# Optimization experiments

Measured on AMD Instinct MI355X. Metric: run time of the kernel, lower is better.

## Reference

```python
import jax, jax.numpy as jnp
import numpy as np

B, Q, S, U = 65536, 128, 8, 32  # batch, n_slices, slice_length (1024/128), hidden units


def setup_inputs() -> dict:
    key = jax.random.key(0)
    k1, k2, k3 = jax.random.split(key, 3)
    x = jax.random.normal(k1, (B, 1, 1, Q * S), dtype=jnp.float32)
    # Per-slice 2-layer MLP params: Dense(U, elu) then Dense(1), one set per slice.
    W1 = jax.random.normal(k2, (Q, S, U), dtype=jnp.float32) * (1.0 / np.sqrt(S))
    b1 = jnp.zeros((Q, U), dtype=jnp.float32)
    W2 = jax.random.normal(k3, (Q, U, 1), dtype=jnp.float32) * (1.0 / np.sqrt(U))
    b2 = jnp.zeros((Q, 1), dtype=jnp.float32)
    return {"x": x, "W1": W1, "b1": b1, "W2": W2, "b2": b2}


def reference(x, W1, b1, W2, b2):
    # x: (B,1,1,C) -> (B, Q, S); note: BN layers in the original __init__ are
    # never used in call(), so the forward is purely the per-slice MLPs.
    b = x.shape[0]
    xs = jnp.reshape(x, (b, Q, S))
    # All 128 per-slice Dense layers fused into one batched GEMM.
    h = jax.nn.elu(jnp.einsum('bqs,qsu->bqu', xs, W1) + b1)  # (B,Q,U)
    out = jnp.einsum('bqu,quo->bqo', h, W2) + b2              # (B,Q,1)
    return jnp.reshape(out, (b, Q))                           # concat over q -> (B,Q)
```

## Files before the change

### kernel.cpp

```cpp
#include <hip/hip_runtime.h>

#define Q    128
#define S    8
#define U    32
#define QW   8
#define TROWS 64
#define RPB  1024
#define NTILE (RPB / TROWS)
#define RSTRIDE 272
#define ZOFF (TROWS * RSTRIDE)
#define OSS  20

typedef __attribute__((ext_vector_type(8)))  __bf16 bf16x8;
typedef __attribute__((ext_vector_type(16))) float  f32x16;
typedef __attribute__((ext_vector_type(2)))  float  f32x2;

__device__ inline unsigned short f2bf(float f) {
    unsigned int u = __float_as_uint(f);
    u += 0x7FFF + ((u >> 16) & 1);
    return (unsigned short)(u >> 16);
}

__device__ inline unsigned int cvt_pk_bf16(float lo, float hi) {
    unsigned int r;
    asm("v_cvt_pk_bf16_f32 %0, %1, %2" : "=v"(r) : "v"(lo), "v"(hi));
    return r;
}

__global__ void prep_kernel(const float* __restrict__ W1, const float* __restrict__ b1,
                            const float* __restrict__ W2, const float* __restrict__ b2,
                            unsigned short* __restrict__ W1T,
                            float* __restrict__ b1F, float* __restrict__ w2F,
                            float* __restrict__ b2F)
{
    const int q = blockIdx.x, t = threadIdx.x;
    const int u = t & 31, s = t >> 5;
    W1T[(q * 32 + u) * 8 + s] = f2bf(W1[(q * 8 + s) * 32 + u]);
    if (t < 32) {
        int reg = t & 15, hh = t >> 4;
        int uu  = (reg & 3) + 8 * (reg >> 2) + 4 * hh;
        b1F[(q * 2 + hh) * 16 + reg] = b1[q * 32 + uu] + 1.0f;
        w2F[(q * 2 + hh) * 16 + reg] = W2[q * 32 + uu];
    }
    if (t == 0) {
        float sw = 0.f;
        for (int uu = 0; uu < 32; ++uu) sw += W2[q * 32 + uu];
        b2F[q] = b2[q] - sw;
    }
}

__global__ __launch_bounds__(256)
__attribute__((amdgpu_waves_per_eu(3, 4)))
void divenc_wreg(const float* __restrict__ x,
                 const unsigned short* __restrict__ W1T,
                 const float* __restrict__ b1F,
                 const float* __restrict__ w2F,
                 const float* __restrict__ b2F,
                 float* __restrict__ out, int B)
{
    __shared__ __align__(16) unsigned char xs[TROWS * RSTRIDE + 16];
    __shared__ __align__(16) float os[TROWS * OSS];

    const int t    = threadIdx.x;
    const int lane = t & 63;
    const int wv   = __builtin_amdgcn_readfirstlane(t >> 6);
    const int bl   = lane & 31;
    const int h    = lane >> 5;
    const bool lo  = (lane < 32);

    const int bid   = blockIdx.x;
    const int qb    = (bid & 15) * QW;
    const int rbase = (bid >> 4) * RPB;
    const int rmax  = B - 1;

    if (t == 0) *(uint4*)(xs + ZOFF) = uint4{0, 0, 0, 0};

    const int qA = qb + wv * 2, qB = qA + 1;
    const uint4  axA  = *(const uint4*)(W1T + ((size_t)qA * 32 + bl) * 8);
    const uint4  axB  = *(const uint4*)(W1T + ((size_t)qB * 32 + bl) * 8);
    const f32x16 cinA = *(const f32x16*)(b1F + ((size_t)qA * 2 + h) * 16);
    const f32x16 cinB = *(const f32x16*)(b1F + ((size_t)qB * 2 + h) * 16);
    const f32x16 wrA  = *(const f32x16*)(w2F + ((size_t)qA * 2 + h) * 16);
    const f32x16 wrB  = *(const f32x16*)(w2F + ((size_t)qB * 2 + h) * 16);
    const float  b2A  = b2F[qA], b2B = b2F[qB];

    const f32x2 l2e2  = 1.44269504088896f;
    const f32x2 nl2e2 = -1.44269504088896f;
    const f32x2 zero2 = 0.0f;

    const int row0 = t >> 3,          qr0 = t & 7;
    const int row1 = (t + 256) >> 3,  qr1 = t & 7;
    float4 pa0, pb0, pa1, pb1;

#define LOADT(T) {                                                                   \
    int r0_ = rbase + (T) * TROWS + row0; if (r0_ > rmax) r0_ = rmax;                \
    int r1_ = rbase + (T) * TROWS + row1; if (r1_ > rmax) r1_ = rmax;                \
    const float4* p0_ = (const float4*)(x + (size_t)r0_ * (Q * S)                    \
                                          + (size_t)(qb + qr0) * S);                 \
    const float4* p1_ = (const float4*)(x + (size_t)r1_ * (Q * S)                    \
                                          + (size_t)(qb + qr1) * S);                 \
    pa0 = p0_[0]; pb0 = p0_[1];                                                      \
    pa1 = p1_[0]; pb1 = p1_[1]; }

#define WRITET() {                                                                   \
    uint4 w0_, w1_;                                                                  \
    w0_.x = cvt_pk_bf16(pa0.x, pa0.y); w0_.y = cvt_pk_bf16(pa0.z, pa0.w);            \
    w0_.z = cvt_pk_bf16(pb0.x, pb0.y); w0_.w = cvt_pk_bf16(pb0.z, pb0.w);            \
    w1_.x = cvt_pk_bf16(pa1.x, pa1.y); w1_.y = cvt_pk_bf16(pa1.z, pa1.w);            \
    w1_.z = cvt_pk_bf16(pb1.x, pb1.y); w1_.w = cvt_pk_bf16(pb1.z, pb1.w);            \
    *(uint4*)(xs + row0 * RSTRIDE + qr0 * 16) = w0_;                                 \
    *(uint4*)(xs + row1 * RSTRIDE + qr1 * 16) = w1_; }

#define EL2(CC, J, WR, ACC) {                                                        \
    f32x2 v_; v_.x = CC[2*(J)]; v_.y = CC[2*(J)+1];                                  \
    f32x2 w2v; w2v.x = WR[2*(J)]; w2v.y = WR[2*(J)+1];                               \
    f32x2 f_ = __builtin_elementwise_fma(v_, l2e2, nl2e2);                           \
    f_ = __builtin_elementwise_min(f_, zero2);                                       \
    f32x2 e_; e_.x = __builtin_amdgcn_exp2f(f_.x);                                   \
    e_.y = __builtin_amdgcn_exp2f(f_.y);                                             \
    f32x2 r_ = __builtin_elementwise_max(v_, e_);                                    \
    ACC = __builtin_elementwise_fma(r_, w2v, ACC); }

#define COMP(AX, CIN, WR, B2, QR) {                                                  \
    const int xoff = bl * RSTRIDE + (QR) * 16;                                       \
    uint4 bx0 = *(const uint4*)(xs + (lo ? xoff                : ZOFF));             \
    uint4 bx1 = *(const uint4*)(xs + (lo ? xoff + 32 * RSTRIDE : ZOFF));             \
    f32x16 cc0 = __builtin_amdgcn_mfma_f32_32x32x16_bf16(                            \
        __builtin_bit_cast(bf16x8, AX), __builtin_bit_cast(bf16x8, bx0),             \
        CIN, 0, 0, 0);                                                               \
    f32x16 cc1 = __builtin_amdgcn_mfma_f32_32x32x16_bf16(                            \
        __builtin_bit_cast(bf16x8, AX), __builtin_bit_cast(bf16x8, bx1),             \
        CIN, 0, 0, 0);                                                               \
    f32x2 acc0 = 0.0f, acc1 = 0.0f;                                                  \
    EL2(cc0, 0, WR, acc0) EL2(cc0, 1, WR, acc0) EL2(cc0, 2, WR, acc0)                \
    EL2(cc0, 3, WR, acc0) EL2(cc0, 4, WR, acc0) EL2(cc0, 5, WR, acc0)                \
    EL2(cc0, 6, WR, acc0) EL2(cc0, 7, WR, acc0)                                      \
    EL2(cc1, 0, WR, acc1) EL2(cc1, 1, WR, acc1) EL2(cc1, 2, WR, acc1)                \
    EL2(cc1, 3, WR, acc1) EL2(cc1, 4, WR, acc1) EL2(cc1, 5, WR, acc1)                \
    EL2(cc1, 6, WR, acc1) EL2(cc1, 7, WR, acc1)                                      \
    float a0 = acc0.x + acc0.y;                                                      \
    float a1 = acc1.x + acc1.y;                                                      \
    a0 += __shfl_xor(a0, 32);                                  \
    a1 += __shfl_xor(a1, 32);                                                        \
    if (lo) {                                                                        \
        os[bl * OSS + (QR)]        = a0 + (B2);                                      \
        os[(bl + 32) * OSS + (QR)] = a1 + (B2);                                      \
    } }

    LOADT(0) WRITET()

    #pragma unroll 1
    for (int tile = 0; tile < NTILE; ++tile) {
        __syncthreads();

        if (tile + 1 < NTILE) LOADT(tile + 1)

        COMP(axA, cinA, wrA, b2A, wv * 2)
        COMP(axB, cinB, wrB, b2B, wv * 2 + 1)

        __syncthreads();

        if (t < 128) {
            int row = t >> 1, c = t & 1;
            float4 o = *(const float4*)&os[row * OSS + c * 4];
            int r = rbase + tile * TROWS + row;
            if (r < B)
                *(float4*)(out + (size_t)r * Q + qb + c * 4) = o;
        }

        if (tile + 1 < NTILE) WRITET()
    }
#undef LOADT
#undef WRITET
#undef EL2
#undef COMP
}

extern "C" void kernel_launch(void* const* d_in, const int* in_sizes, int n_in,
                              void* d_out, int out_size, void* d_ws, size_t ws_size,
                              hipStream_t stream) {
    const float* x  = (const float*)d_in[0];
    const float* W1 = (const float*)d_in[1];
    const float* b1 = (const float*)d_in[2];
    const float* W2 = (const float*)d_in[3];
    const float* b2 = (const float*)d_in[4];
    float* out = (float*)d_out;

    unsigned short* W1T = (unsigned short*)d_ws;
    float*          b1F = (float*)((char*)d_ws + 65536);
    float*          w2F = (float*)((char*)d_ws + 81920);
    float*          b2F = (float*)((char*)d_ws + 98304);

    const int B = in_sizes[0] / (Q * S);
    const int nblocks = ((B + RPB - 1) / RPB) * (Q / QW);

    hipLaunchKernelGGL(prep_kernel, dim3(Q), dim3(256), 0, stream,
                       W1, b1, W2, b2, W1T, b1F, w2F, b2F);
    hipLaunchKernelGGL(divenc_wreg, dim3(nblocks), dim3(256), 0, stream,
                       x, W1T, b1F, w2F, b2F, out, B);
}
```

Measured before the change: 82.16 us.

## Double-buffer x and output tiles in LDS to drop one barrier per tile

The staged input tile and output tile in shared memory become double-buffered, so the next tile can be written while the current one is computed and the previous tile's outputs are stored. This removes the second __syncthreads per iteration and defers each output store by one iteration. The LDS row stride also shrinks from 272 to 144 bytes, which keeps the total footprint modest but may change bank-conflict behaviour on the MFMA operand reads.

```diff
diff --git a/kernel.cpp b/kernel.cpp
--- a/kernel.cpp
+++ b/kernel.cpp
@@ -7,9 +7,11 @@
 #define TROWS 64
 #define RPB  1024
 #define NTILE (RPB / TROWS)
-#define RSTRIDE 272
-#define ZOFF (TROWS * RSTRIDE)
-#define OSS  20
+#define RSTRIDE 144
+#define XSBUF (TROWS * RSTRIDE)
+#define ZOFF  (2 * XSBUF)
+#define OSS   20
+#define OSBUF (TROWS * OSS)
 
 typedef __attribute__((ext_vector_type(8)))  __bf16 bf16x8;
 typedef __attribute__((ext_vector_type(16))) float  f32x16;
@@ -58,8 +60,8 @@
                  const float* __restrict__ b2F,
                  float* __restrict__ out, int B)
 {
-    __shared__ __align__(16) unsigned char xs[TROWS * RSTRIDE + 16];
-    __shared__ __align__(16) float os[TROWS * OSS];
+    __shared__ __align__(16) unsigned char xs[2 * XSBUF + 16];
+    __shared__ __align__(16) float os[2 * OSBUF];
 
     const int t    = threadIdx.x;
     const int lane = t & 63;
@@ -102,14 +104,14 @@
     pa0 = p0_[0]; pb0 = p0_[1];                                                      \
     pa1 = p1_[0]; pb1 = p1_[1]; }
 
-#define WRITET() {                                                                   \
+#define WRITET(BUF) {                                                                \
     uint4 w0_, w1_;                                                                  \
     w0_.x = cvt_pk_bf16(pa0.x, pa0.y); w0_.y = cvt_pk_bf16(pa0.z, pa0.w);            \
     w0_.z = cvt_pk_bf16(pb0.x, pb0.y); w0_.w = cvt_pk_bf16(pb0.z, pb0.w);            \
     w1_.x = cvt_pk_bf16(pa1.x, pa1.y); w1_.y = cvt_pk_bf16(pa1.z, pa1.w);            \
     w1_.z = cvt_pk_bf16(pb1.x, pb1.y); w1_.w = cvt_pk_bf16(pb1.z, pb1.w);            \
-    *(uint4*)(xs + row0 * RSTRIDE + qr0 * 16) = w0_;                                 \
-    *(uint4*)(xs + row1 * RSTRIDE + qr1 * 16) = w1_; }
+    *(uint4*)(xs + (BUF) * XSBUF + row0 * RSTRIDE + qr0 * 16) = w0_;                 \
+    *(uint4*)(xs + (BUF) * XSBUF + row1 * RSTRIDE + qr1 * 16) = w1_; }
 
 #define EL2(CC, J, WR, ACC) {                                                        \
     f32x2 v_; v_.x = CC[2*(J)]; v_.y = CC[2*(J)+1];                                  \
@@ -121,8 +123,8 @@
     f32x2 r_ = __builtin_elementwise_max(v_, e_);                                    \
     ACC = __builtin_elementwise_fma(r_, w2v, ACC); }
 
-#define COMP(AX, CIN, WR, B2, QR) {                                                  \
-    const int xoff = bl * RSTRIDE + (QR) * 16;                                       \
+#define COMP(AX, CIN, WR, B2, QR, RBUF, OSP) {                                       \
+    const int xoff = (RBUF) + bl * RSTRIDE + (QR) * 16;                              \
     uint4 bx0 = *(const uint4*)(xs + (lo ? xoff                : ZOFF));             \
     uint4 bx1 = *(const uint4*)(xs + (lo ? xoff + 32 * RSTRIDE : ZOFF));             \
     f32x16 cc0 = __builtin_amdgcn_mfma_f32_32x32x16_bf16(                            \
@@ -143,37 +145,43 @@
     a0 += __shfl_xor(a0, 32);                                  \
     a1 += __shfl_xor(a1, 32);                                                        \
     if (lo) {                                                                        \
-        os[bl * OSS + (QR)]        = a0 + (B2);                                      \
-        os[(bl + 32) * OSS + (QR)] = a1 + (B2);                                      \
+        os[(OSP) + bl * OSS + (QR)]        = a0 + (B2);                              \
+        os[(OSP) + (bl + 32) * OSS + (QR)] = a1 + (B2);                              \
     } }
 
-    LOADT(0) WRITET()
+#define STORE(T, OSP) {                                                              \
+    if (t < 128) {                                                                   \
+        int row_ = t >> 1, c_ = t & 1;                                               \
+        float4 o_ = *(const float4*)&os[(OSP) + row_ * OSS + c_ * 4];                \
+        int r_ = rbase + (T) * TROWS + row_;                                         \
+        if (r_ < B)                                                                  \
+            *(float4*)(out + (size_t)r_ * Q + qb + c_ * 4) = o_;                     \
+    } }
+
+    LOADT(0) WRITET(0)
 
     #pragma unroll 1
     for (int tile = 0; tile < NTILE; ++tile) {
         __syncthreads();
+        const int rbuf = (tile & 1) * XSBUF;
+        const int osp  = (tile & 1) * OSBUF;
+        const int psp  = ((tile & 1) ^ 1) * OSBUF;
 
         if (tile + 1 < NTILE) LOADT(tile + 1)
-
-        COMP(axA, cinA, wrA, b2A, wv * 2)
-        COMP(axB, cinB, wrB, b2B, wv * 2 + 1)
-
-        __syncthreads();
-
-        if (t < 128) {
-            int row = t >> 1, c = t & 1;
-            float4 o = *(const float4*)&os[row * OSS + c * 4];
-            int r = rbase + tile * TROWS + row;
-            if (r < B)
-                *(float4*)(out + (size_t)r * Q + qb + c * 4) = o;
-        }
-
-        if (tile + 1 < NTILE) WRITET()
+        if (tile > 0)         STORE(tile - 1, psp)
+
+        COMP(axA, cinA, wrA, b2A, wv * 2,     rbuf, osp)
+        COMP(axB, cinB, wrB, b2B, wv * 2 + 1, rbuf, osp)
+
+        if (tile + 1 < NTILE) WRITET((tile + 1) & 1)
     }
+    __syncthreads();
+    STORE(NTILE - 1, ((NTILE - 1) & 1) * OSBUF)
 #undef LOADT
 #undef WRITET
 #undef EL2
 #undef COMP
+#undef STORE
 }
 
 extern "C" void kernel_launch(void* const* d_in, const int* in_sizes, int n_in,
```

New measurement: 89.86 us. +9.4%, slower.
